# Performance work log

Measured on AMD Instinct MI355X. Metric: run time of the kernel, lower is better.

The kernel has to match this reference:

```python
import jax, jax.numpy as jnp
import numpy as np

PRESERVE_RATIO = 0.8
TEMPERATURE = 1.5


def setup_inputs() -> dict:
    key = jax.random.key(0)
    ks = jax.random.split(key, 8)
    B, C, H, W = 2, 64, 96, 96
    inter = C // 2
    bott = C // 4
    s = 0.02
    return {
        "x": jax.random.normal(ks[0], (B, C, H, W), dtype=jnp.float32),
        "g_w": jax.random.normal(ks[1], (inter, C), dtype=jnp.float32) * s,
        "theta_w": jax.random.normal(ks[2], (inter, C), dtype=jnp.float32) * s,
        "phi_w": jax.random.normal(ks[3], (inter, C), dtype=jnp.float32) * s,
        "W_w": jax.random.normal(ks[4], (C, inter), dtype=jnp.float32) * s,
        "cg1_w": jax.random.normal(ks[5], (bott, C), dtype=jnp.float32) * s,
        "cg1_b": jnp.zeros((bott,), dtype=jnp.float32),
        "cg2_w": jax.random.normal(ks[6], (C, bott), dtype=jnp.float32) * s,
        "cg2_b": jnp.zeros((C,), dtype=jnp.float32),
    }


def reference(x, g_w, theta_w, phi_w, W_w, cg1_w, cg1_b, cg2_w, cg2_b):
    B, C, H, W = x.shape
    N = H * W
    # color gate: global avg pool -> 1x1 conv -> relu -> 1x1 conv -> sigmoid
    pooled = jnp.mean(x, axis=(2, 3))                       # [B, C]
    h = jax.nn.relu(pooled @ cg1_w.T + cg1_b)               # [B, C//4]
    gate = jax.nn.sigmoid(h @ cg2_w.T + cg2_b)              # [B, C]

    xf = x.reshape(B, C, N)                                 # [B, C, N]
    g_x = jnp.einsum('ic,bcn->bni', g_w, xf)                # [B, N, I]
    theta = jnp.einsum('ic,bcn->bni', theta_w, xf)          # [B, N, I]
    phi = jnp.einsum('ic,bcn->bin', phi_w, xf)              # [B, I, N]

    affinity = jnp.einsum('bni,bim->bnm', theta, phi) / TEMPERATURE  # [B, N, N]
    affinity = jax.nn.softmax(affinity, axis=-1)
    y = jnp.einsum('bnm,bmi->bni', affinity, g_x)           # [B, N, I]
    y = jnp.einsum('ci,bni->bcn', W_w, y).reshape(B, C, H, W)
    y = y * gate[:, :, None, None] * PRESERVE_RATIO
    return x + y
```

## Files before the change

### kernel.cpp

```cpp
#include <hip/hip_runtime.h>

#define N_TOK 9216
#define C_DIM 64
#define I_DIM 32
#define BOT 16
#define B_SZ 2
#define N_TILES 144

typedef short bf16x8 __attribute__((ext_vector_type(8)));
typedef float f32x4 __attribute__((ext_vector_type(4)));
typedef float f32x16 __attribute__((ext_vector_type(16)));

__device__ __forceinline__ unsigned packbf(float a, float b) {
  return __builtin_amdgcn_perm(__float_as_uint(b), __float_as_uint(a), 0x07060302u);
}
__device__ __forceinline__ unsigned short bftrunc(float f) {
  return (unsigned short)(__float_as_uint(f) >> 16);
}

__global__ __launch_bounds__(256) void pool_kernel(const float* __restrict__ x,
                                                   float* __restrict__ pooled) {
  int bc = blockIdx.x;
  const float* p = x + (size_t)bc * N_TOK;
  float s = 0.f;
  for (int t = threadIdx.x; t < N_TOK; t += 256) s += p[t];
#pragma unroll
  for (int off = 32; off >= 1; off >>= 1) s += __shfl_down(s, off, 64);
  __shared__ float red[4];
  int wid = threadIdx.x >> 6, lane = threadIdx.x & 63;
  if (lane == 0) red[wid] = s;
  __syncthreads();
  if (threadIdx.x == 0)
    pooled[bc] = (red[0] + red[1] + red[2] + red[3]) * (1.0f / N_TOK);
}

__global__ __launch_bounds__(256) void proj_kernel(
    const float* __restrict__ x, const float* __restrict__ g_w,
    const float* __restrict__ theta_w, const float* __restrict__ phi_w,
    unsigned short* __restrict__ Q, unsigned short* __restrict__ K,
    unsigned short* __restrict__ VT) {
  const int lane = threadIdx.x & 63;
  const int m = lane & 15, quad = lane >> 4;
  int task = blockIdx.x * 4 + (threadIdx.x >> 6);
  int mat = task / 1152;
  int r0 = task % 1152;
  int b = r0 / 576;
  int n0 = (r0 % 576) * 16;
  const float* wsrc = (mat == 0) ? theta_w : ((mat == 1) ? phi_w : g_w);
  const float scale = (mat == 0) ? 0.96179669439f : 1.0f;

  bf16x8 afr[2][2];
#pragma unroll
  for (int it = 0; it < 2; ++it)
#pragma unroll
    for (int cs = 0; cs < 2; ++cs) {
      const float* wp = wsrc + (it * 16 + m) * C_DIM + cs * 32 + quad * 8;
      union { unsigned u[4]; bf16x8 v; } t;
#pragma unroll
      for (int j = 0; j < 4; ++j)
        t.u[j] = packbf(wp[2 * j] * scale, wp[2 * j + 1] * scale);
      afr[it][cs] = t.v;
    }

  const float* xb = x + (size_t)b * C_DIM * N_TOK + n0 + m;
  bf16x8 bfr[2];
#pragma unroll
  for (int cs = 0; cs < 2; ++cs) {
    union { unsigned u[4]; bf16x8 v; } t;
#pragma unroll
    for (int j = 0; j < 4; ++j) {
      float v0 = xb[(size_t)(cs * 32 + quad * 8 + 2 * j) * N_TOK];
      float v1 = xb[(size_t)(cs * 32 + quad * 8 + 2 * j + 1) * N_TOK];
      t.u[j] = packbf(v0, v1);
    }
    bfr[cs] = t.v;
  }

  f32x4 acc[2] = {{0.f, 0.f, 0.f, 0.f}, {0.f, 0.f, 0.f, 0.f}};
#pragma unroll
  for (int cs = 0; cs < 2; ++cs)
#pragma unroll
    for (int it = 0; it < 2; ++it)
      acc[it] = __builtin_amdgcn_mfma_f32_16x16x32_bf16(afr[it][cs], bfr[cs],
                                                        acc[it], 0, 0, 0);
  if (mat < 2) {
    unsigned short* dst =
        ((mat == 0) ? Q : K) + ((size_t)b * N_TOK + n0 + m) * I_DIM;
#pragma unroll
    for (int it = 0; it < 2; ++it) {
      unsigned u0 = packbf(acc[it][0], acc[it][1]);
      unsigned u1 = packbf(acc[it][2], acc[it][3]);
      *(uint2*)(dst + it * 16 + quad * 4) = make_uint2(u0, u1);
    }
  } else {
#pragma unroll
    for (int it = 0; it < 2; ++it)
#pragma unroll
      for (int r = 0; r < 4; ++r)
        VT[((size_t)b * I_DIM + it * 16 + quad * 4 + r) * N_TOK + n0 + m] =
            bftrunc(acc[it][r]);
  }
}

__global__ __launch_bounds__(256, 4) void attn_kernel(
    const unsigned short* __restrict__ Q, const unsigned short* __restrict__ Kg,
    const unsigned short* __restrict__ VT, float* __restrict__ Ypart,
    float* __restrict__ Lpart, int tps) {
  const int lane = threadIdx.x & 63;
  const int l32 = lane & 31, h = lane >> 5;
  const int wid = threadIdx.x >> 6;
  const int qw = blockIdx.x * 4 + wid;
  const int ks = blockIdx.y, b = blockIdx.z;
  const int q0 = qw * 32;
  const unsigned short* Qb = Q + (size_t)b * N_TOK * I_DIM;
  const unsigned short* Kb = Kg + (size_t)b * N_TOK * I_DIM;
  const unsigned short* Vb = VT + (size_t)b * I_DIM * N_TOK;

  __shared__ __align__(16) unsigned short Pw[4][32][68];
  unsigned short(*P)[68] = Pw[wid];

  bf16x8 bq0 = *(const bf16x8*)(Qb + (size_t)(q0 + l32) * I_DIM + h * 8);
  bf16x8 bq1 = *(const bf16x8*)(Qb + (size_t)(q0 + l32) * I_DIM + 16 + h * 8);

  const f32x16 zz = {};
  f32x16 accy = {};
  float lsum = 0.f;

  const int kt0 = ks * tps;
  for (int kt = kt0; kt < kt0 + tps; ++kt) {
    const int k0 = kt * 64;
    const unsigned short* kp = Kb + (size_t)(k0 + l32) * I_DIM + h * 8;
    bf16x8 ak00 = *(const bf16x8*)(kp);
    bf16x8 ak01 = *(const bf16x8*)(kp + 16);
    bf16x8 ak10 = *(const bf16x8*)(kp + 32 * I_DIM);
    bf16x8 ak11 = *(const bf16x8*)(kp + 32 * I_DIM + 16);
    const unsigned short* vp = Vb + (size_t)l32 * N_TOK + k0 + h * 8;
    bf16x8 bv[4];
    bv[0] = *(const bf16x8*)(vp);
    bv[1] = *(const bf16x8*)(vp + 16);
    bv[2] = *(const bf16x8*)(vp + 32);
    bv[3] = *(const bf16x8*)(vp + 48);

    f32x16 s0 = __builtin_amdgcn_mfma_f32_32x32x16_bf16(ak00, bq0, zz, 0, 0, 0);
    s0 = __builtin_amdgcn_mfma_f32_32x32x16_bf16(ak01, bq1, s0, 0, 0, 0);
    f32x16 s1 = __builtin_amdgcn_mfma_f32_32x32x16_bf16(ak10, bq0, zz, 0, 0, 0);
    s1 = __builtin_amdgcn_mfma_f32_32x32x16_bf16(ak11, bq1, s1, 0, 0, 0);

#pragma unroll
    for (int t = 0; t < 2; ++t) {
      const f32x16 sv = t ? s1 : s0;
      float e[16];
#pragma unroll
      for (int r = 0; r < 16; ++r) {
        e[r] = __builtin_amdgcn_exp2f(sv[r]);
        lsum += e[r];
      }
      unsigned pk[8];
#pragma unroll
      for (int i = 0; i < 8; ++i) pk[i] = packbf(e[2 * i], e[2 * i + 1]);
      unsigned short* row = &P[l32][t * 32 + 4 * h];
      *(uint2*)(row) = make_uint2(pk[0], pk[1]);
      *(uint2*)(row + 8) = make_uint2(pk[2], pk[3]);
      *(uint2*)(row + 16) = make_uint2(pk[4], pk[5]);
      *(uint2*)(row + 24) = make_uint2(pk[6], pk[7]);
    }

#pragma unroll
    for (int s = 0; s < 4; ++s) {
      union { uint2 d[2]; bf16x8 v; } ap;
      const unsigned short* rp = &P[l32][16 * s + 8 * h];
      ap.d[0] = *(const uint2*)(rp);
      ap.d[1] = *(const uint2*)(rp + 4);
      accy = __builtin_amdgcn_mfma_f32_32x32x16_bf16(ap.v, bv[s], accy, 0, 0, 0);
    }
  }

  lsum += __shfl_xor(lsum, 32, 64);

  const size_t base = (size_t)(ks * B_SZ + b) * N_TOK + q0;
#pragma unroll
  for (int R = 0; R < 4; ++R)
#pragma unroll
    for (int r = 0; r < 4; ++r)
      Ypart[(base + r + 8 * R + 4 * h) * I_DIM + l32] = accy[4 * R + r];
  if (h == 0) Lpart[base + l32] = lsum;
}

__global__ __launch_bounds__(256) void epilogue_kernel(
    const float* __restrict__ x, const float* __restrict__ W_w,
    const float* __restrict__ pooled, const float* __restrict__ cg1_w,
    const float* __restrict__ cg1_b, const float* __restrict__ cg2_w,
    const float* __restrict__ cg2_b, const float* __restrict__ Ypart,
    const float* __restrict__ Lpart, float* __restrict__ out, int KS) {
  __shared__ float Ysh[64][33];
  __shared__ float lsh[64];
  __shared__ float gsh[64];
  __shared__ float hl[BOT];
  const int t = threadIdx.x;
  const int b = blockIdx.y;
  const int n0 = blockIdx.x * 64;

  if (t < BOT) {
    float a = cg1_b[t];
#pragma unroll
    for (int c = 0; c < C_DIM; ++c)
      a += cg1_w[t * C_DIM + c] * pooled[b * C_DIM + c];
    hl[t] = a > 0.f ? a : 0.f;
  }

  {
    int nl = t >> 2, i0 = (t & 3) * 8;
    float4 s0 = make_float4(0.f, 0.f, 0.f, 0.f), s1 = s0;
    for (int ks = 0; ks < KS; ++ks) {
      const float* yp =
          Ypart + ((size_t)(ks * B_SZ + b) * N_TOK + n0 + nl) * I_DIM + i0;
      float4 v0 = *(const float4*)(yp);
      float4 v1 = *(const float4*)(yp + 4);
      s0.x += v0.x; s0.y += v0.y; s0.z += v0.z; s0.w += v0.w;
      s1.x += v1.x; s1.y += v1.y; s1.z += v1.z; s1.w += v1.w;
    }
    Ysh[nl][i0 + 0] = s0.x; Ysh[nl][i0 + 1] = s0.y;
    Ysh[nl][i0 + 2] = s0.z; Ysh[nl][i0 + 3] = s0.w;
    Ysh[nl][i0 + 4] = s1.x; Ysh[nl][i0 + 5] = s1.y;
    Ysh[nl][i0 + 6] = s1.z; Ysh[nl][i0 + 7] = s1.w;
    if (t < 64) {
      float ls = 0.f;
      for (int ks = 0; ks < KS; ++ks)
        ls += Lpart[(size_t)(ks * B_SZ + b) * N_TOK + n0 + t];
      lsh[t] = ls;
    }
  }
  __syncthreads();

  if (t < C_DIM) {
    float z = cg2_b[t];
#pragma unroll
    for (int j = 0; j < BOT; ++j) z += cg2_w[t * BOT + j] * hl[j];
    gsh[t] = 0.8f / (1.f + __expf(-z));
  }
  __syncthreads();

  const int n = t & 63, cg = t >> 6;
  float y[I_DIM];
#pragma unroll
  for (int i = 0; i < I_DIM; ++i) y[i] = Ysh[n][i];
  const float inv = 1.0f / lsh[n];
  const float* xb = x + ((size_t)b * C_DIM + cg * 16) * N_TOK + n0 + n;
  float* ob = out + ((size_t)b * C_DIM + cg * 16) * N_TOK + n0 + n;
#pragma unroll
  for (int c16 = 0; c16 < 16; ++c16) {
    const int c = cg * 16 + c16;
    float sacc = 0.f;
#pragma unroll
    for (int i = 0; i < I_DIM; ++i) sacc += W_w[c * I_DIM + i] * y[i];
    ob[(size_t)c16 * N_TOK] = xb[(size_t)c16 * N_TOK] + gsh[c] * inv * sacc;
  }
}

extern "C" void kernel_launch(void* const* d_in, const int* in_sizes, int n_in,
                              void* d_out, int out_size, void* d_ws, size_t ws_size,
                              hipStream_t stream) {
  const float* x = (const float*)d_in[0];
  const float* g_w = (const float*)d_in[1];
  const float* theta_w = (const float*)d_in[2];
  const float* phi_w = (const float*)d_in[3];
  const float* W_w = (const float*)d_in[4];
  const float* cg1_w = (const float*)d_in[5];
  const float* cg1_b = (const float*)d_in[6];
  const float* cg2_w = (const float*)d_in[7];
  const float* cg2_b = (const float*)d_in[8];
  float* out = (float*)d_out;

  char* w = (char*)d_ws;
  const size_t bfsz = (size_t)B_SZ * N_TOK * I_DIM * sizeof(unsigned short);
  unsigned short* Qb = (unsigned short*)(w);
  unsigned short* Kb = (unsigned short*)(w + bfsz);
  unsigned short* VT = (unsigned short*)(w + 2 * bfsz);
  float* pooled = (float*)(w + 3 * bfsz);
  char* w2 = w + 3 * bfsz + 1024;

  int KS = 8;
  {
    const size_t per = (size_t)B_SZ * N_TOK * sizeof(float) * (I_DIM + 1);
    while (KS > 1 && (3 * bfsz + 1024 + (size_t)KS * per) > ws_size) KS >>= 1;
  }
  float* Lpart = (float*)w2;
  float* Ypart = (float*)(w2 + (size_t)KS * B_SZ * N_TOK * sizeof(float));
  int tps = N_TILES / KS;

  proj_kernel<<<dim3(864), 256, 0, stream>>>(x, g_w, theta_w, phi_w, Qb, Kb, VT);
  pool_kernel<<<dim3(B_SZ * C_DIM), 256, 0, stream>>>(x, pooled);
  attn_kernel<<<dim3(72, KS, B_SZ), 256, 0, stream>>>(Qb, Kb, VT, Ypart, Lpart, tps);
  epilogue_kernel<<<dim3(N_TOK / 64, B_SZ), 256, 0, stream>>>(
      x, W_w, pooled, cg1_w, cg1_b, cg2_w, cg2_b, Ypart, Lpart, out, KS);
}
```

Baseline: 173.6 us.

## Keep softmax probabilities in registers, prefetch K/V tiles, fuse pooling into projection

In the attention inner loop, P no longer round-trips through shared memory. The exp results are packed to bf16 and rearranged across wave halves with v_permlane32_swap so they can feed the P·V MFMA directly as the A operand. K and V tiles are now software double-buffered, so the next tile's loads are issued before the current tile's MFMAs and exps. The row-sum uses four partial accumulators instead of one serial chain, and the pooling kernel is folded into the projection launch as extra blocks to save a launch. The risks are a wrong lane mapping from the permlane swap, an assumption that tps is even, and prefetch reads one tile past each split's range.

```diff
diff --git a/kernel.cpp b/kernel.cpp
--- a/kernel.cpp
+++ b/kernel.cpp
@@ -18,27 +18,26 @@
   return (unsigned short)(__float_as_uint(f) >> 16);
 }
 
-__global__ __launch_bounds__(256) void pool_kernel(const float* __restrict__ x,
-                                                   float* __restrict__ pooled) {
-  int bc = blockIdx.x;
-  const float* p = x + (size_t)bc * N_TOK;
-  float s = 0.f;
-  for (int t = threadIdx.x; t < N_TOK; t += 256) s += p[t];
-#pragma unroll
-  for (int off = 32; off >= 1; off >>= 1) s += __shfl_down(s, off, 64);
-  __shared__ float red[4];
-  int wid = threadIdx.x >> 6, lane = threadIdx.x & 63;
-  if (lane == 0) red[wid] = s;
-  __syncthreads();
-  if (threadIdx.x == 0)
-    pooled[bc] = (red[0] + red[1] + red[2] + red[3]) * (1.0f / N_TOK);
-}
-
-__global__ __launch_bounds__(256) void proj_kernel(
+__global__ __launch_bounds__(256) void proj_pool_kernel(
     const float* __restrict__ x, const float* __restrict__ g_w,
     const float* __restrict__ theta_w, const float* __restrict__ phi_w,
     unsigned short* __restrict__ Q, unsigned short* __restrict__ K,
-    unsigned short* __restrict__ VT) {
+    unsigned short* __restrict__ VT, float* __restrict__ pooled) {
+  if (blockIdx.x >= 864) {
+    int bc = blockIdx.x - 864;
+    const float* p = x + (size_t)bc * N_TOK;
+    float s = 0.f;
+    for (int t = threadIdx.x; t < N_TOK; t += 256) s += p[t];
+#pragma unroll
+    for (int off = 32; off >= 1; off >>= 1) s += __shfl_down(s, off, 64);
+    __shared__ float red[4];
+    int wid = threadIdx.x >> 6, lane = threadIdx.x & 63;
+    if (lane == 0) red[wid] = s;
+    __syncthreads();
+    if (threadIdx.x == 0)
+      pooled[bc] = (red[0] + red[1] + red[2] + red[3]) * (1.0f / N_TOK);
+    return;
+  }
   const int lane = threadIdx.x & 63;
   const int m = lane & 15, quad = lane >> 4;
   int task = blockIdx.x * 4 + (threadIdx.x >> 6);
@@ -102,77 +101,96 @@
   }
 }
 
+__device__ __forceinline__ void tilework(const f32x16 s, const bf16x8 bvA,
+                                         const bf16x8 bvB, f32x16& accy,
+                                         float& lsum) {
+  float e[16];
+#pragma unroll
+  for (int r = 0; r < 16; ++r) e[r] = __builtin_amdgcn_exp2f(s[r]);
+  float l0 = 0.f, l1 = 0.f, l2 = 0.f, l3 = 0.f;
+#pragma unroll
+  for (int r = 0; r < 4; ++r) {
+    l0 += e[r]; l1 += e[4 + r]; l2 += e[8 + r]; l3 += e[12 + r];
+  }
+  lsum += (l0 + l1) + (l2 + l3);
+  unsigned pk[8];
+#pragma unroll
+  for (int i = 0; i < 8; ++i) pk[i] = packbf(e[2 * i], e[2 * i + 1]);
+  asm("v_permlane32_swap_b32 %0, %1" : "+v"(pk[0]), "+v"(pk[2]));
+  asm("v_permlane32_swap_b32 %0, %1" : "+v"(pk[1]), "+v"(pk[3]));
+  asm("v_permlane32_swap_b32 %0, %1" : "+v"(pk[4]), "+v"(pk[6]));
+  asm("v_permlane32_swap_b32 %0, %1" : "+v"(pk[5]), "+v"(pk[7]));
+  union { unsigned u[4]; bf16x8 v; } A0, A1;
+  A0.u[0] = pk[0]; A0.u[1] = pk[1]; A0.u[2] = pk[2]; A0.u[3] = pk[3];
+  A1.u[0] = pk[4]; A1.u[1] = pk[5]; A1.u[2] = pk[6]; A1.u[3] = pk[7];
+  accy = __builtin_amdgcn_mfma_f32_32x32x16_bf16(A0.v, bvA, accy, 0, 0, 0);
+  accy = __builtin_amdgcn_mfma_f32_32x32x16_bf16(A1.v, bvB, accy, 0, 0, 0);
+}
+
+__device__ __forceinline__ void attn_step(const bf16x8 bq0, const bf16x8 bq1,
+                                          bf16x8 cak[4], bf16x8 cbv[4],
+                                          bf16x8 nak[4], bf16x8 nbv[4],
+                                          const unsigned short*& kp,
+                                          const unsigned short*& vp,
+                                          f32x16& accy, float& lsum) {
+  const f32x16 zz = {};
+  kp += 64 * I_DIM;
+  vp += 64;
+  nak[0] = *(const bf16x8*)(kp);
+  nak[1] = *(const bf16x8*)(kp + 16);
+  nak[2] = *(const bf16x8*)(kp + 32 * I_DIM);
+  nak[3] = *(const bf16x8*)(kp + 32 * I_DIM + 16);
+  nbv[0] = *(const bf16x8*)(vp);
+  nbv[1] = *(const bf16x8*)(vp + 16);
+  nbv[2] = *(const bf16x8*)(vp + 32);
+  nbv[3] = *(const bf16x8*)(vp + 48);
+
+  f32x16 s0 = __builtin_amdgcn_mfma_f32_32x32x16_bf16(cak[0], bq0, zz, 0, 0, 0);
+  s0 = __builtin_amdgcn_mfma_f32_32x32x16_bf16(cak[1], bq1, s0, 0, 0, 0);
+  f32x16 s1 = __builtin_amdgcn_mfma_f32_32x32x16_bf16(cak[2], bq0, zz, 0, 0, 0);
+  s1 = __builtin_amdgcn_mfma_f32_32x32x16_bf16(cak[3], bq1, s1, 0, 0, 0);
+
+  tilework(s0, cbv[0], cbv[1], accy, lsum);
+  tilework(s1, cbv[2], cbv[3], accy, lsum);
+}
+
 __global__ __launch_bounds__(256, 4) void attn_kernel(
     const unsigned short* __restrict__ Q, const unsigned short* __restrict__ Kg,
     const unsigned short* __restrict__ VT, float* __restrict__ Ypart,
     float* __restrict__ Lpart, int tps) {
   const int lane = threadIdx.x & 63;
   const int l32 = lane & 31, h = lane >> 5;
-  const int wid = threadIdx.x >> 6;
-  const int qw = blockIdx.x * 4 + wid;
+  const int qw = blockIdx.x * 4 + (threadIdx.x >> 6);
   const int ks = blockIdx.y, b = blockIdx.z;
   const int q0 = qw * 32;
   const unsigned short* Qb = Q + (size_t)b * N_TOK * I_DIM;
   const unsigned short* Kb = Kg + (size_t)b * N_TOK * I_DIM;
   const unsigned short* Vb = VT + (size_t)b * I_DIM * N_TOK;
 
-  __shared__ __align__(16) unsigned short Pw[4][32][68];
-  unsigned short(*P)[68] = Pw[wid];
-
   bf16x8 bq0 = *(const bf16x8*)(Qb + (size_t)(q0 + l32) * I_DIM + h * 8);
   bf16x8 bq1 = *(const bf16x8*)(Qb + (size_t)(q0 + l32) * I_DIM + 16 + h * 8);
 
-  const f32x16 zz = {};
   f32x16 accy = {};
   float lsum = 0.f;
 
   const int kt0 = ks * tps;
-  for (int kt = kt0; kt < kt0 + tps; ++kt) {
-    const int k0 = kt * 64;
-    const unsigned short* kp = Kb + (size_t)(k0 + l32) * I_DIM + h * 8;
-    bf16x8 ak00 = *(const bf16x8*)(kp);
-    bf16x8 ak01 = *(const bf16x8*)(kp + 16);
-    bf16x8 ak10 = *(const bf16x8*)(kp + 32 * I_DIM);
-    bf16x8 ak11 = *(const bf16x8*)(kp + 32 * I_DIM + 16);
-    const unsigned short* vp = Vb + (size_t)l32 * N_TOK + k0 + h * 8;
-    bf16x8 bv[4];
-    bv[0] = *(const bf16x8*)(vp);
-    bv[1] = *(const bf16x8*)(vp + 16);
-    bv[2] = *(const bf16x8*)(vp + 32);
-    bv[3] = *(const bf16x8*)(vp + 48);
-
-    f32x16 s0 = __builtin_amdgcn_mfma_f32_32x32x16_bf16(ak00, bq0, zz, 0, 0, 0);
-    s0 = __builtin_amdgcn_mfma_f32_32x32x16_bf16(ak01, bq1, s0, 0, 0, 0);
-    f32x16 s1 = __builtin_amdgcn_mfma_f32_32x32x16_bf16(ak10, bq0, zz, 0, 0, 0);
-    s1 = __builtin_amdgcn_mfma_f32_32x32x16_bf16(ak11, bq1, s1, 0, 0, 0);
-
-#pragma unroll
-    for (int t = 0; t < 2; ++t) {
-      const f32x16 sv = t ? s1 : s0;
-      float e[16];
-#pragma unroll
-      for (int r = 0; r < 16; ++r) {
-        e[r] = __builtin_amdgcn_exp2f(sv[r]);
-        lsum += e[r];
-      }
-      unsigned pk[8];
-#pragma unroll
-      for (int i = 0; i < 8; ++i) pk[i] = packbf(e[2 * i], e[2 * i + 1]);
-      unsigned short* row = &P[l32][t * 32 + 4 * h];
-      *(uint2*)(row) = make_uint2(pk[0], pk[1]);
-      *(uint2*)(row + 8) = make_uint2(pk[2], pk[3]);
-      *(uint2*)(row + 16) = make_uint2(pk[4], pk[5]);
-      *(uint2*)(row + 24) = make_uint2(pk[6], pk[7]);
-    }
-
-#pragma unroll
-    for (int s = 0; s < 4; ++s) {
-      union { uint2 d[2]; bf16x8 v; } ap;
-      const unsigned short* rp = &P[l32][16 * s + 8 * h];
-      ap.d[0] = *(const uint2*)(rp);
-      ap.d[1] = *(const uint2*)(rp + 4);
-      accy = __builtin_amdgcn_mfma_f32_32x32x16_bf16(ap.v, bv[s], accy, 0, 0, 0);
-    }
+  const unsigned short* kp = Kb + ((size_t)kt0 * 64 + l32) * I_DIM + h * 8;
+  const unsigned short* vp = Vb + (size_t)l32 * N_TOK + kt0 * 64 + h * 8;
+
+  bf16x8 ak[4], bv[4], nak[4], nbv[4];
+  ak[0] = *(const bf16x8*)(kp);
+  ak[1] = *(const bf16x8*)(kp + 16);
+  ak[2] = *(const bf16x8*)(kp + 32 * I_DIM);
+  ak[3] = *(const bf16x8*)(kp + 32 * I_DIM + 16);
+  bv[0] = *(const bf16x8*)(vp);
+  bv[1] = *(const bf16x8*)(vp + 16);
+  bv[2] = *(const bf16x8*)(vp + 32);
+  bv[3] = *(const bf16x8*)(vp + 48);
+
+  const int half = tps >> 1;
+  for (int it = 0; it < half; ++it) {
+    attn_step(bq0, bq1, ak, bv, nak, nbv, kp, vp, accy, lsum);
+    attn_step(bq0, bq1, nak, nbv, ak, bv, kp, vp, accy, lsum);
   }
 
   lsum += __shfl_xor(lsum, 32, 64);
@@ -277,19 +295,19 @@
   unsigned short* Kb = (unsigned short*)(w + bfsz);
   unsigned short* VT = (unsigned short*)(w + 2 * bfsz);
   float* pooled = (float*)(w + 3 * bfsz);
-  char* w2 = w + 3 * bfsz + 1024;
+  char* w2 = w + 3 * bfsz + 4096;
 
   int KS = 8;
   {
     const size_t per = (size_t)B_SZ * N_TOK * sizeof(float) * (I_DIM + 1);
-    while (KS > 1 && (3 * bfsz + 1024 + (size_t)KS * per) > ws_size) KS >>= 1;
+    while (KS > 1 && (3 * bfsz + 4096 + (size_t)KS * per) > ws_size) KS >>= 1;
   }
   float* Lpart = (float*)w2;
   float* Ypart = (float*)(w2 + (size_t)KS * B_SZ * N_TOK * sizeof(float));
   int tps = N_TILES / KS;
 
-  proj_kernel<<<dim3(864), 256, 0, stream>>>(x, g_w, theta_w, phi_w, Qb, Kb, VT);
-  pool_kernel<<<dim3(B_SZ * C_DIM), 256, 0, stream>>>(x, pooled);
+  proj_pool_kernel<<<dim3(992), 256, 0, stream>>>(x, g_w, theta_w, phi_w, Qb,
+                                                  Kb, VT, pooled);
   attn_kernel<<<dim3(72, KS, B_SZ), 256, 0, stream>>>(Qb, Kb, VT, Ypart, Lpart, tps);
   epilogue_kernel<<<dim3(N_TOK / 64, B_SZ), 256, 0, stream>>>(
       x, W_w, pooled, cg1_w, cg1_b, cg2_w, cg2_b, Ypart, Lpart, out, KS);
```

After: 176.3 us. No clear change (+1.5%).
